# Performance work log

Hardware: AMD Instinct MI355X
Metric: run time of the kernel (lower is better)

The kernel has to match this reference:

```python
import jax, jax.numpy as jnp
import numpy as np


def _selective_scan(u, delta, A, Bm, Cm, Dskip, delta_bias):
    # u, delta: (B, K*D, L); A: (K*D, N); Bm, Cm: (B, K, N, L); Dskip, delta_bias: (K*D,)
    Bsz, KD, L = u.shape
    K = Bm.shape[1]
    D = KD // K
    N = A.shape[1]
    dt = jax.nn.softplus(delta + delta_bias[None, :, None])          # (B,KD,L)
    u4 = u.reshape(Bsz, K, D, L)
    dt4 = dt.reshape(Bsz, K, D, L)
    A4 = A.reshape(K, D, N)
    # discretization: dA = exp(dt*A), dBu = dt * B * u
    dA = jnp.exp(dt4[..., None] * A4[None, :, :, None, :])            # (B,K,D,L,N)
    Bt = jnp.transpose(Bm, (0, 1, 3, 2))                               # (B,K,L,N)
    dBu = dt4[..., None] * u4[..., None] * Bt[:, :, None, :, :]        # (B,K,D,L,N)
    dA_l = jnp.moveaxis(dA, 3, 0)                                      # (L,B,K,D,N)
    dBu_l = jnp.moveaxis(dBu, 3, 0)

    def step(h, ab):
        a, b = ab
        h = a * h + b
        return h, h

    h0 = jnp.zeros(dA_l.shape[1:], dA.dtype)
    _, hs = jax.lax.scan(step, h0, (dA_l, dBu_l))                      # (L,B,K,D,N)
    C_l = jnp.moveaxis(Cm, 3, 0)                                       # (L,B,K,N)
    y = jnp.einsum('lbkdn,lbkn->lbkd', hs, C_l)                        # (L,B,K,D)
    y = jnp.moveaxis(y, 0, 3).reshape(Bsz, KD, L)
    return y + u * Dskip[None, :, None]


def setup_inputs() -> dict:
    key = jax.random.key(0)
    ks = jax.random.split(key, 8)
    B, H, W, C = 2, 64, 64, 96
    Di, N, K = 192, 16, 4
    R = 6  # ceil(96/16)
    x = jax.random.normal(ks[0], (B, H, W, C), jnp.float32)
    in_proj_w = jax.random.normal(ks[1], (2 * Di, C), jnp.float32) * (C ** -0.5)
    conv_w = jax.random.normal(ks[2], (Di, 1, 3, 3), jnp.float32) * 0.2
    conv_b = jax.random.normal(ks[3], (Di,), jnp.float32) * 0.02
    x_proj_weight = jax.random.normal(ks[4], (K, R + 2 * N, Di), jnp.float32) * (Di ** -0.5)
    dt_projs_weight = jax.random.uniform(ks[5], (K, Di, R), jnp.float32, -(R ** -0.5), R ** -0.5)
    dt = jnp.exp(jax.random.uniform(ks[6], (K, Di), jnp.float32) * (np.log(0.1) - np.log(0.001)) + np.log(0.001))
    dt = jnp.clip(dt, 1e-4)
    dt_projs_bias = dt + jnp.log(-jnp.expm1(-dt))                      # inverse softplus
    A_logs = jnp.log(jnp.tile(jnp.arange(1, N + 1, dtype=jnp.float32), (K * Di, 1)))
    Ds = jnp.ones((K * Di,), jnp.float32)
    out_norm_w = jnp.ones((Di,), jnp.float32)
    out_norm_b = jnp.zeros((Di,), jnp.float32)
    out_proj_w = jax.random.normal(ks[7], (C, Di), jnp.float32) * (Di ** -0.5)
    return dict(x=x, in_proj_w=in_proj_w, conv_w=conv_w, conv_b=conv_b,
                x_proj_weight=x_proj_weight, dt_projs_weight=dt_projs_weight,
                dt_projs_bias=dt_projs_bias, A_logs=A_logs, Ds=Ds,
                out_norm_w=out_norm_w, out_norm_b=out_norm_b, out_proj_w=out_proj_w)


def reference(x, in_proj_w, conv_w, conv_b, x_proj_weight, dt_projs_weight,
              dt_projs_bias, A_logs, Ds, out_norm_w, out_norm_b, out_proj_w):
    Bsz, H, W, C = x.shape
    Di = conv_w.shape[0]
    K = x_proj_weight.shape[0]
    R = dt_projs_weight.shape[2]
    N = A_logs.shape[1]
    L = H * W
    # in_proj (bias=False) and split into x, z
    xz = x @ in_proj_w.T                                               # (B,H,W,2*Di)
    xi, z = jnp.split(xz, 2, axis=-1)
    # depthwise conv2d + SiLU (channel-first)
    xc = jnp.transpose(xi, (0, 3, 1, 2))                               # (B,Di,H,W)
    xc = jax.lax.conv_general_dilated(xc, conv_w, (1, 1), 'SAME',
                                      feature_group_count=Di) + conv_b[None, :, None, None]
    xc = jax.nn.silu(xc)
    # cross-scan: 4 directions (row-major, col-major, and their reverses)
    x0 = xc.reshape(Bsz, Di, L)
    x1 = jnp.transpose(xc, (0, 1, 3, 2)).reshape(Bsz, Di, L)
    xs = jnp.stack([x0, x1, x0[..., ::-1], x1[..., ::-1]], axis=1)      # (B,K,Di,L)
    # per-direction projections
    x_dbl = jnp.einsum('bkdl,kcd->bkcl', xs, x_proj_weight)            # (B,K,R+2N,L)
    dts, Bs, Cs = jnp.split(x_dbl, [R, R + N], axis=2)
    dts = jnp.einsum('bkrl,kdr->bkdl', dts, dt_projs_weight)           # (B,K,Di,L)
    A = -jnp.exp(A_logs)                                               # (K*Di,N)
    ys = _selective_scan(xs.reshape(Bsz, K * Di, L), dts.reshape(Bsz, K * Di, L),
                         A, Bs, Cs, Ds, dt_projs_bias.reshape(-1))
    ys = ys.reshape(Bsz, K, Di, L)
    # cross-merge
    y = ys[:, 0] + ys[:, 2, :, ::-1]
    yt = ys[:, 1] + ys[:, 3, :, ::-1]                                  # col-major ordering
    y = y + jnp.transpose(yt.reshape(Bsz, Di, W, H), (0, 1, 3, 2)).reshape(Bsz, Di, L)
    y = jnp.transpose(y.reshape(Bsz, Di, H, W), (0, 2, 3, 1))          # (B,H,W,Di)
    # out_norm: LayerNorm over channel
    mu = jnp.mean(y, axis=-1, keepdims=True)
    var = jnp.mean((y - mu) ** 2, axis=-1, keepdims=True)
    y = (y - mu) * jax.lax.rsqrt(var + 1e-5) * out_norm_w + out_norm_b
    # gate and out_proj (bias=False)
    y = y * jax.nn.silu(z)
    return y @ out_proj_w.T
```

## Files before the change

kernel.cpp:

```cpp
#include <hip/hip_runtime.h>
#include <hip/hip_fp16.h>
#include <math.h>


static constexpr int Bsz = 2;
static constexpr int Lc  = 4096;
static constexpr int Cc  = 96;
static constexpr int Dd  = 192;
static constexpr int Kk  = 4;
static constexpr int NC  = 32;

__device__ __forceinline__ float bu(unsigned short v) {
    return __uint_as_float((unsigned int)v << 16);
}
__device__ __forceinline__ unsigned short f2b(float f) {
    unsigned int u = __float_as_uint(f);
    return (unsigned short)((u + 0x7fffu + ((u >> 16) & 1u)) >> 16);
}

template<int CTRL>
__device__ __forceinline__ float dppadd(float x) {
    return x + __int_as_float(__builtin_amdgcn_update_dpp(
        0, __float_as_int(x), CTRL, 0xf, 0xf, true));
}
__device__ __forceinline__ float red16(float x) {
    x = dppadd<0xB1>(x);
    x = dppadd<0x4E>(x);
    x = dppadd<0x124>(x);
    x = dppadd<0x128>(x);
    return x;
}

__global__ __launch_bounds__(256) void k0_detect(const unsigned short* __restrict__ x,
                                                 int* __restrict__ flag)
{
    __shared__ int s[256];
    int cnt = 0;
    for (int i = threadIdx.x; i < 4096; i += 256) {
        int e = (x[i] >> 7) & 0xFF;
        cnt += (e >= 118 && e <= 131) ? 1 : 0;
    }
    s[threadIdx.x] = cnt;
    __syncthreads();
    for (int st = 128; st > 0; st >>= 1) {
        if (threadIdx.x < st) s[threadIdx.x] += s[threadIdx.x + st];
        __syncthreads();
    }
    if (threadIdx.x == 0) flag[0] = (s[0] >= 3072) ? 1 : 0;
}

struct Cv {
    const void* src[12];
    int off[12];
    int n[12];
};
__global__ __launch_bounds__(256) void k0b_convert(Cv cv, const int* __restrict__ flag,
                                                   float* __restrict__ dstbase)
{
    int bf = flag[0];
    int t = blockIdx.y;
    int i = blockIdx.x * 256 + threadIdx.x;
    if (i >= cv.n[t]) return;
    if (t == 11) {
        int cp = i % 40;
        int d  = (i / 40) % 192;
        int k  = i / 7680;
        float v = 0.f;
        if (cp < 38) {
            size_t si = (size_t)(k * 38 + cp) * 192 + d;
            v = bf ? bu(((const unsigned short*)cv.src[11])[si])
                   : ((const float*)cv.src[11])[si];
        }
        dstbase[cv.off[11] + i] = v;
        return;
    }
    float v;
    if (bf) v = bu(((const unsigned short*)cv.src[t])[i]);
    else    v = ((const float*)cv.src[t])[i];
    dstbase[cv.off[t] + i] = v;
}

__global__ __launch_bounds__(256) void k1_inproj(const void* __restrict__ xraw,
                                                 const int* __restrict__ flag,
                                                 const float* __restrict__ wf,
                                                 float* __restrict__ xiT, __half* __restrict__ zT)
{
    __shared__ float xT[64 * 97];
    const int bf = flag[0];
    int lt = blockIdx.x & 127;
    int jq = blockIdx.x >> 7;
    int row0 = lt * 64;
    for (int e = threadIdx.x; e < 64 * 96; e += 256) {
        int i = e / 96, c = e % 96;
        size_t idx = (size_t)(row0 + i) * Cc + c;
        xT[i * 97 + c] = bf ? bu(((const unsigned short*)xraw)[idx])
                            : ((const float*)xraw)[idx];
    }
    __syncthreads();
    int pi = threadIdx.x & 63;
    int q  = __builtin_amdgcn_readfirstlane(threadIdx.x >> 6);
    int j0 = jq * 96 + q * 24;
    float acc[24];
#pragma unroll
    for (int j = 0; j < 24; ++j) acc[j] = 0.f;
    for (int c4 = 0; c4 < 24; ++c4) {
        float xv0 = xT[pi * 97 + c4 * 4 + 0];
        float xv1 = xT[pi * 97 + c4 * 4 + 1];
        float xv2 = xT[pi * 97 + c4 * 4 + 2];
        float xv3 = xT[pi * 97 + c4 * 4 + 3];
#pragma unroll
        for (int j = 0; j < 24; ++j) {
            float4 w4 = *reinterpret_cast<const float4*>(&wf[(size_t)(j0 + j) * 96 + c4 * 4]);
            acc[j] += w4.x * xv0 + w4.y * xv1 + w4.z * xv2 + w4.w * xv3;
        }
    }
    int b = row0 >> 12;
    int l = (row0 & 4095) + pi;
    if (jq < 2) {
#pragma unroll
        for (int j = 0; j < 24; ++j)
            xiT[((size_t)b * Dd + j0 + j) * Lc + l] = acc[j];
    } else {
#pragma unroll
        for (int j = 0; j < 24; ++j) {
            float v = acc[j];
            zT[((size_t)b * Dd + (j0 + j - 192)) * Lc + l] =
                __float2half(v / (1.f + __expf(-v)));
        }
    }
}

__global__ __launch_bounds__(256) void k2b_conv(const float* __restrict__ xiT,
                                                const float* __restrict__ cwf,
                                                const float* __restrict__ cbf,
                                                float* __restrict__ xc,
                                                float* __restrict__ uT)
{
    __shared__ float inl[34 * 66];
    __shared__ float outl[32 * 65];
    int bid = blockIdx.x;
    int half = bid & 1;
    int d = (bid >> 1) % Dd;
    int b = bid / (2 * Dd);
    int h0 = half * 32;
    const float* src = xiT + (size_t)(b * Dd + d) * Lc;
    for (int r = threadIdx.x; r < 34; r += 256) {
        inl[r * 66 + 0] = 0.f;
        inl[r * 66 + 65] = 0.f;
    }
    for (int e = threadIdx.x; e < 34 * 64; e += 256) {
        int row = e >> 6, w = e & 63;
        int h = h0 - 1 + row;
        inl[row * 66 + 1 + w] = (h >= 0 && h < 64) ? src[h * 64 + w] : 0.f;
    }
    __syncthreads();
    float wgt[9];
#pragma unroll
    for (int t = 0; t < 9; t++) wgt[t] = cwf[d * 9 + t];
    float bias = cbf[d];
    int hs = threadIdx.x >> 6, w = threadIdx.x & 63;
    float* dstrow = xc + (size_t)(b * Dd + d) * Lc;
#pragma unroll
    for (int it = 0; it < 8; ++it) {
        int hh = it * 4 + hs;
        float acc = bias;
#pragma unroll
        for (int dy = 0; dy < 3; ++dy) {
            const float* rp = &inl[(hh + dy) * 66 + w];
#pragma unroll
            for (int dx = 0; dx < 3; ++dx)
                acc += rp[dx] * wgt[dy * 3 + dx];
        }
        float s = acc / (1.f + __expf(-acc));
        dstrow[(h0 + hh) * 64 + w] = s;
        outl[hh * 65 + w] = s;
    }
    __syncthreads();
    float* udst = uT + (size_t)(b * Dd + d) * Lc;
    for (int e = threadIdx.x; e < 2048; e += 256) {
        int w2 = e >> 5, hh2 = e & 31;
        udst[w2 * 64 + h0 + hh2] = outl[hh2 * 65 + w2];
    }
}

__global__ __launch_bounds__(256) void k3_proj(const float* __restrict__ xc,
                                               const float* __restrict__ uT,
                                               const float* __restrict__ Wg,
                                               const float* __restrict__ dtwf,
                                               const float* __restrict__ dtbf,
                                               __half* __restrict__ dtH,
                                               float* __restrict__ BsT, float* __restrict__ CsT)
{
    __shared__ float xL[192 * 64];
    __shared__ float rawdt[6][64];
    int bid = blockIdx.x;
    int pt = bid & 63, k = (bid >> 6) & 3, b = bid >> 8;
    int s0 = pt * 64;
    const float* xb = ((k & 1) ? uT : xc) + (size_t)b * Dd * Lc + s0;
    for (int e = threadIdx.x; e < 3072; e += 256) {
        int d = e >> 4, c4 = e & 15;
        *reinterpret_cast<float4*>(&xL[d * 64 + c4 * 4]) =
            *reinterpret_cast<const float4*>(xb + (size_t)d * Lc + c4 * 4);
    }
    __syncthreads();

    int pi = threadIdx.x & 63;
    int q  = __builtin_amdgcn_readfirstlane(threadIdx.x >> 6);

    const float* wk = Wg + (size_t)k * 192 * 40 + q * 10;

    float acc[10];
#pragma unroll
    for (int j = 0; j < 10; ++j) acc[j] = 0.f;

    for (int d = 0; d < 192; ++d) {
        float xv = xL[d * 64 + pi];
        const float* wrow = wk + d * 40;
#pragma unroll
        for (int j = 0; j < 10; ++j) acc[j] += wrow[j] * xv;
    }

    if (q == 0) {
#pragma unroll
        for (int j = 0; j < 6; ++j) rawdt[j][pi] = acc[j];
    }
    size_t bk16 = (size_t)(b * Kk + k) * 16;
#pragma unroll
    for (int j = 0; j < 10; ++j) {
        int cp = q * 10 + j;
        if (cp >= 6 && cp < 22)
            BsT[(bk16 + (cp - 6)) * Lc + s0 + pi] = acc[j];
        else if (cp >= 22 && cp < 38)
            CsT[(bk16 + (cp - 22)) * Lc + s0 + pi] = acc[j];
    }
    __syncthreads();

    float raws[6];
#pragma unroll
    for (int r = 0; r < 6; ++r) raws[r] = rawdt[r][pi];
    const float* dtw = dtwf + (size_t)(k * 192 + q * 48) * 6;
    const float* dtb = dtbf + k * 192 + q * 48;
    __half* dto = dtH + ((size_t)(b * Kk + k) * Dd + q * 48) * Lc + s0 + pi;
    for (int dd = 0; dd < 48; ++dd) {
        float s = dtb[dd];
#pragma unroll
        for (int r = 0; r < 6; ++r) s += raws[r] * dtw[dd * 6 + r];
        float sp = fmaxf(s, 0.f) + __logf(1.f + __expf(-fabsf(s)));
        dto[(size_t)dd * Lc] = __float2half(sp);
    }
}

template<int REV, int PASS3>
__device__ __forceinline__ void scan_run(const float* __restrict__ ubase,
                                         const __half* __restrict__ dbase,
                                         const float* __restrict__ Bbase,
                                         const float* __restrict__ Cbase,
                                         float* uL, float* bL, float* cL, __half* dL,
                                         int dl, int n, int c,
                                         float An,
                                         float* __restrict__ P, float* __restrict__ S,
                                         size_t pidx, __half* __restrict__ yrow)
{
    const int t0 = c * 128;
    const int mb0 = REV ? (Lc - 64 - t0) : t0;
    const int mb1 = REV ? (Lc - 128 - t0) : (t0 + 64);

    float4 ru = *reinterpret_cast<const float4*>(ubase + mb0 + n * 4);
    float4 rb = *reinterpret_cast<const float4*>(Bbase + mb0 + n * 4);
    float4 rc{};
    if (PASS3) rc = *reinterpret_cast<const float4*>(Cbase + mb0 + n * 4);
    uint2 rd = *reinterpret_cast<const uint2*>(dbase + mb0 + n * 4);
    *reinterpret_cast<float4*>(uL + dl * 68 + n * 4) = ru;
    *reinterpret_cast<float4*>(bL + dl * 68 + n * 4) = rb;
    if (PASS3) *reinterpret_cast<float4*>(cL + dl * 68 + n * 4) = rc;
    *reinterpret_cast<uint2*>(dL + dl * 72 + n * 4) = rd;
    __syncthreads();

    ru = *reinterpret_cast<const float4*>(ubase + mb1 + n * 4);
    rb = *reinterpret_cast<const float4*>(Bbase + mb1 + n * 4);
    if (PASS3) rc = *reinterpret_cast<const float4*>(Cbase + mb1 + n * 4);
    rd = *reinterpret_cast<const uint2*>(dbase + mb1 + n * 4);

    float h = PASS3 ? P[pidx] : 0.f;
    float sdt = 0.f, ystash = 0.f;

#define SS2D_HALF(HH)                                                           \
    {                                                                           \
        _Pragma("unroll 4")                                                     \
        for (int qi = 0; qi < 16; ++qi) {                                       \
            const int col4 = REV ? (60 - qi * 4) : (qi * 4);                    \
            float4 uq = *reinterpret_cast<const float4*>(uL + dl * 68 + col4);  \
            float4 bq = *reinterpret_cast<const float4*>(bL + n * 68 + col4);   \
            float4 cq{};                                                        \
            if (PASS3) cq = *reinterpret_cast<const float4*>(cL + n * 68 + col4);\
            uint2 dq = *reinterpret_cast<const uint2*>(dL + dl * 72 + col4);    \
            const __half2* dh2 = reinterpret_cast<const __half2*>(&dq);         \
            _Pragma("unroll")                                                   \
            for (int j = 0; j < 4; ++j) {                                       \
                const int e = REV ? (3 - j) : j;                                \
                float dtv = (e & 1) ? __high2float(dh2[e >> 1])                 \
                                    : __low2float(dh2[e >> 1]);                 \
                float uv = reinterpret_cast<const float*>(&uq)[e];              \
                float bv = reinterpret_cast<const float*>(&bq)[e];              \
                float a = __expf(dtv * An);                                     \
                if (!PASS3) sdt += dtv;                                         \
                h = a * h + (dtv * uv) * bv;                                    \
                if (PASS3) {                                                    \
                    float cv = reinterpret_cast<const float*>(&cq)[e];          \
                    float yv = red16(h * cv);                                   \
                    const int i15 = (qi & 3) * 4 + j;                           \
                    if (i15 == n) ystash = yv;                                  \
                    if (i15 == 15) {                                            \
                        int tb = t0 + (HH) * 64 + (qi >> 2) * 16 + n;           \
                        int aw = REV ? (Lc - 1 - tb) : tb;                      \
                        yrow[aw] = __float2half(ystash);                        \
                    }                                                           \
                }                                                               \
            }                                                                   \
        }                                                                       \
    }

    SS2D_HALF(0);
    __syncthreads();
    *reinterpret_cast<float4*>(uL + dl * 68 + n * 4) = ru;
    *reinterpret_cast<float4*>(bL + dl * 68 + n * 4) = rb;
    if (PASS3) *reinterpret_cast<float4*>(cL + dl * 68 + n * 4) = rc;
    *reinterpret_cast<uint2*>(dL + dl * 72 + n * 4) = rd;
    __syncthreads();
    SS2D_HALF(1);
#undef SS2D_HALF

    if (!PASS3) {
        P[pidx] = __expf(An * sdt);
        S[pidx] = h;
    }
}

template<int PASS3>
__global__ __launch_bounds__(256) void kscan(const __half* __restrict__ dtH,
                                             const float* __restrict__ xc,
                                             const float* __restrict__ uT,
                                             const float* __restrict__ BsT,
                                             const float* __restrict__ CsT,
                                             const float* __restrict__ alogf,
                                             float* __restrict__ P,
                                             float* __restrict__ S,
                                             __half* __restrict__ ysH)
{
    __shared__ float uL[16 * 68];
    __shared__ float bL[16 * 68];
    __shared__ float cL[PASS3 ? 16 * 68 : 4];
    __shared__ __half dL[16 * 72];

    int c  = blockIdx.x & 31;
    int t1 = blockIdx.x >> 5;
    int dg = t1 % 12;
    int kk = (t1 / 12) & 3;
    int b  = t1 / 48;
    int n  = threadIdx.x & 15, dl = threadIdx.x >> 4;
    int d  = dg * 16 + dl;

    const float* ubz = ((kk & 1) ? uT : xc) + (size_t)b * Dd * Lc;
    const float*  ubase = ubz + (size_t)d * Lc;
    const __half* dbase = dtH + ((size_t)((b * Kk + kk) * Dd + d)) * Lc;
    const float*  Bbase = BsT + ((size_t)((b * Kk + kk) * 16 + dl)) * Lc;
    const float*  Cbase = CsT + ((size_t)((b * Kk + kk) * 16 + dl)) * Lc;

    float An  = -__expf(alogf[(kk * Dd + d) * 16 + n]);
    size_t pidx = (((size_t)(b * Kk + kk) * Dd + d) * NC + c) * 16 + n;
    __half* yrow = PASS3 ? ysH + ((size_t)(kk * Bsz + b) * Dd + d) * Lc : nullptr;

    if (kk >= 2)
        scan_run<1, PASS3>(ubase, dbase, Bbase, Cbase, uL, bL, cL, dL,
                           dl, n, c, An, P, S, pidx, yrow);
    else
        scan_run<0, PASS3>(ubase, dbase, Bbase, Cbase, uL, bL, cL, dL,
                           dl, n, c, An, P, S, pidx, yrow);
}

__global__ __launch_bounds__(64) void k6_pass2(float* __restrict__ P, const float* __restrict__ S)
{
    int g = blockIdx.x * 64 + threadIdx.x;
    int n = g & 15;
    int chain = g >> 4;
    size_t base = (size_t)chain * NC * 16 + n;
    float h = 0.f;
#pragma unroll
    for (int c = 0; c < NC; ++c) {
        size_t id = base + (size_t)c * 16;
        float p = P[id], s = S[id];
        P[id] = h;
        h = p * h + s;
    }
}

__global__ __launch_bounds__(256) void k8t(const __half* __restrict__ ysH,
                                           __half* __restrict__ ysT)
{
    __shared__ float t[64 * 65];
    int bid = blockIdx.x;
    int d = bid % Dd, b = bid / Dd;
    const __half* y1 = ysH + ((size_t)(1 * Bsz + b) * Dd + d) * Lc;
    const __half* y3 = ysH + ((size_t)(3 * Bsz + b) * Dd + d) * Lc;
    __half* dst = ysT + ((size_t)b * Dd + d) * Lc;
    for (int e = threadIdx.x; e < 4096; e += 256)
        t[(e >> 6) * 65 + (e & 63)] = __half2float(y1[e]) + __half2float(y3[e]);
    __syncthreads();
    for (int e = threadIdx.x; e < 4096; e += 256)
        dst[e] = __float2half(t[(e & 63) * 65 + (e >> 6)]);
}

__global__ __launch_bounds__(256) void k8_norm(const __half* __restrict__ ysH,
                                               const __half* __restrict__ ysT,
                                               const __half* __restrict__ zT,
                                               const float* __restrict__ xc,
                                               const float* __restrict__ dsf,
                                               const float* __restrict__ nwf,
                                               const float* __restrict__ nbf,
                                               __half* __restrict__ gH)
{
    __shared__ float yt[192 * 33];
    __shared__ float ps1[8 * 32], ps2[8 * 32];
    __shared__ float mu[32], rs[32];
    int bid = blockIdx.x;
    int pt = bid & 127, b = bid >> 7;
    int p0 = pt * 32;
    for (int e = threadIdx.x; e < 192 * 32; e += 256) {
        int d = e >> 5, p = e & 31;
        size_t r0 = ((size_t)(0 * Bsz + b) * Dd + d) * Lc + p0 + p;
        size_t r2 = ((size_t)(2 * Bsz + b) * Dd + d) * Lc + p0 + p;
        size_t rt = ((size_t)b * Dd + d) * Lc + p0 + p;
        float ds4 = dsf[d] + dsf[192 + d] + dsf[384 + d] + dsf[576 + d];
        yt[d * 33 + p] = __half2float(ysH[r0]) + __half2float(ysH[r2])
                       + __half2float(ysT[rt])
                       + xc[((size_t)b * Dd + d) * Lc + p0 + p] * ds4;
    }
    __syncthreads();
    {
        int p = threadIdx.x & 31, q = threadIdx.x >> 5;
        float s1 = 0.f, s2 = 0.f;
        for (int dd = 0; dd < 24; ++dd) {
            float v = yt[(q * 24 + dd) * 33 + p];
            s1 += v; s2 += v * v;
        }
        ps1[q * 32 + p] = s1; ps2[q * 32 + p] = s2;
    }
    __syncthreads();
    if (threadIdx.x < 32) {
        int p = threadIdx.x;
        float s1 = 0.f, s2 = 0.f;
        for (int q = 0; q < 8; ++q) { s1 += ps1[q * 32 + p]; s2 += ps2[q * 32 + p]; }
        float m = s1 * (1.f / 192.f);
        float var = s2 * (1.f / 192.f) - m * m;
        mu[p] = m; rs[p] = rsqrtf(var + 1e-5f);
    }
    __syncthreads();
    for (int e = threadIdx.x; e < 192 * 32; e += 256) {
        int d = e >> 5, p = e & 31;
        float v = (yt[d * 33 + p] - mu[p]) * rs[p] * nwf[d] + nbf[d];
        float zv = __half2float(zT[((size_t)b * Dd + d) * Lc + p0 + p]);
        yt[d * 33 + p] = v * zv;
    }
    __syncthreads();
    for (int i = threadIdx.x; i < 32 * 192; i += 256) {
        int p = i / 192, d = i - p * 192;
        gH[((size_t)b * Lc + p0 + p) * Dd + d] = __float2half(yt[d * 33 + p]);
    }
}

__global__ __launch_bounds__(1024) void k10_outproj(const __half* __restrict__ gH,
                                                    const float* __restrict__ wof,
                                                    const int* __restrict__ flag,
                                                    void* __restrict__ outv)
{
    __shared__ float gLT[192 * 66];
    const int bf = flag[0];
    int r0 = blockIdx.x * 64;
    for (int e = threadIdx.x; e < 1536; e += 1024) {
        int row = e / 24, j = e % 24;
        __half2 g2[4];
        *reinterpret_cast<uint4*>(g2) =
            *reinterpret_cast<const uint4*>(gH + (size_t)(r0 + row) * Dd + j * 8);
#pragma unroll
        for (int i = 0; i < 4; ++i) {
            gLT[(j * 8 + 2 * i + 0) * 66 + row] = __low2float(g2[i]);
            gLT[(j * 8 + 2 * i + 1) * 66 + row] = __high2float(g2[i]);
        }
    }
    __syncthreads();
    int row = threadIdx.x & 63;
    int w = __builtin_amdgcn_readfirstlane(threadIdx.x >> 6);
    int c0 = w * 6;
    const float* wr = wof + (size_t)c0 * Dd;
    float acc[6];
#pragma unroll
    for (int i = 0; i < 6; ++i) acc[i] = 0.f;
    for (int d = 0; d < 192; ++d) {
        float gv = gLT[d * 66 + row];
#pragma unroll
        for (int cc = 0; cc < 6; ++cc) acc[cc] += wr[(size_t)cc * Dd + d] * gv;
    }
    size_t ob = (size_t)(r0 + row) * Cc + c0;
    if (bf) {
        unsigned short* o = (unsigned short*)outv;
#pragma unroll
        for (int cc = 0; cc < 6; ++cc) o[ob + cc] = f2b(acc[cc]);
    } else {
        float* o = (float*)outv;
#pragma unroll
        for (int cc = 0; cc < 6; ++cc) o[ob + cc] = acc[cc];
    }
}

extern "C" void kernel_launch(void* const* d_in, const int* in_sizes, int n_in,
                              void* d_out, int out_size, void* d_ws, size_t ws_size,
                              hipStream_t stream)
{
    (void)out_size; (void)ws_size;
    float* ws = (float*)d_ws;
    int* flag = (int*)ws;

    int off[12]; int tot = 64;
    off[0] = 0;
    for (int i = 1; i < 12; ++i) {
        off[i] = tot;
        int n = (i < n_in) ? in_sizes[i] : 0;
        tot += (n + 63) & ~63;
    }
    float* winf = ws + off[1];
    float* cwf  = ws + off[2];
    float* cbf  = ws + off[3];
    float* dtwf = ws + off[5];
    float* dtbf = ws + off[6];
    float* alogf= ws + off[7];
    float* dsf  = ws + off[8];
    float* nwf  = ws + off[9];
    float* nbf  = ws + off[10];
    float* wof  = ws + off[11];

    const size_t BASE = 131072;
    __half* dtH = (__half*)(ws + BASE);
    float*  xc  = ws + BASE + 3145728;
    float*  uT  = ws + BASE + 4718592;
    float*  BsT = ws + BASE + 6291456;
    float*  CsT = ws + BASE + 6815744;
    float*  P   = ws + BASE + 7340032;
    float*  S   = ws + BASE + 8126464;
    __half* zT  = (__half*)(ws + BASE + 8912896);
    float*  xiT = ws + BASE + 9699328;
    __half* ysH = (__half*)(ws + BASE + 9699328);
    __half* ysT = (__half*)P;
    __half* gH  = (__half*)S;
    float*  Wg  = ws + BASE + 12845056;

    Cv cv2;
    for (int i = 0; i < 11; ++i) {
        int t = i + 1;
        cv2.src[i] = (t < n_in) ? d_in[t] : d_in[0];
        cv2.off[i] = off[t];
        cv2.n[i]   = (t < n_in) ? in_sizes[t] : 0;
    }
    cv2.src[11] = (4 < n_in) ? d_in[4] : d_in[0];
    cv2.off[11] = (int)(BASE + 12845056);
    cv2.n[11]   = 4 * 192 * 40;

    k0_detect   <<<dim3(1),    dim3(256), 0, stream>>>((const unsigned short*)d_in[0], flag);
    k0b_convert <<<dim3(144, 12), dim3(256), 0, stream>>>(cv2, flag, ws);
    k1_inproj   <<<dim3(512),  dim3(256), 0, stream>>>(d_in[0], flag, winf, xiT, zT);
    k2b_conv    <<<dim3(768),  dim3(256), 0, stream>>>(xiT, cwf, cbf, xc, uT);
    k3_proj     <<<dim3(512),  dim3(256), 0, stream>>>(xc, uT, Wg, dtwf, dtbf, dtH, BsT, CsT);
    kscan<0>    <<<dim3(3072), dim3(256), 0, stream>>>(dtH, xc, uT, BsT, CsT, alogf, P, S, ysH);
    k6_pass2    <<<dim3(384),  dim3(64),  0, stream>>>(P, S);
    kscan<1>    <<<dim3(3072), dim3(256), 0, stream>>>(dtH, xc, uT, BsT, CsT, alogf, P, S, ysH);
    k8t         <<<dim3(384),  dim3(256), 0, stream>>>(ysH, ysT);
    k8_norm     <<<dim3(256),  dim3(256), 0, stream>>>(ysH, ysT, zT, xc, dsf, nwf, nbf, gH);
    k10_outproj <<<dim3(128),  dim3(1024), 0, stream>>>(gH, wof, flag, d_out);
}
```

Measured before the change: 182.5 us.

## Fuse dtype detection into convert and merge layernorm with out-projection

The standalone dtype-detection kernel is folded into the weight-convert kernel, where every block redundantly counts exponents and block 0 writes the flag. The LayerNorm/gating kernel and the output-projection GEMM are merged into one kernel. It works on 64-position tiles held in shared memory, and each wave computes 24 output channels. This removes two launches and the fp16 round trip of the gated activations through global memory. In exchange there are only 128 blocks with 24 accumulators per thread and 50KB of LDS, which lowers occupancy and parallelism for the projection.

```diff
diff --git a/kernel.cpp b/kernel.cpp
--- a/kernel.cpp
+++ b/kernel.cpp
@@ -31,22 +31,23 @@
     return x;
 }
 
-__global__ __launch_bounds__(256) void k0_detect(const unsigned short* __restrict__ x,
-                                                 int* __restrict__ flag)
-{
-    __shared__ int s[256];
+__device__ __forceinline__ int detect_bf(const unsigned short* __restrict__ x,
+                                         int* __restrict__ sbuf)
+{
     int cnt = 0;
     for (int i = threadIdx.x; i < 4096; i += 256) {
         int e = (x[i] >> 7) & 0xFF;
         cnt += (e >= 118 && e <= 131) ? 1 : 0;
     }
-    s[threadIdx.x] = cnt;
+    sbuf[threadIdx.x] = cnt;
     __syncthreads();
     for (int st = 128; st > 0; st >>= 1) {
-        if (threadIdx.x < st) s[threadIdx.x] += s[threadIdx.x + st];
+        if (threadIdx.x < st) sbuf[threadIdx.x] += sbuf[threadIdx.x + st];
         __syncthreads();
     }
-    if (threadIdx.x == 0) flag[0] = (s[0] >= 3072) ? 1 : 0;
+    int r = (sbuf[0] >= 3072) ? 1 : 0;
+    __syncthreads();
+    return r;
 }
 
 struct Cv {
@@ -54,10 +55,13 @@
     int off[12];
     int n[12];
 };
-__global__ __launch_bounds__(256) void k0b_convert(Cv cv, const int* __restrict__ flag,
+__global__ __launch_bounds__(256) void k0b_convert(Cv cv, const unsigned short* __restrict__ xraw,
+                                                   int* __restrict__ flag,
                                                    float* __restrict__ dstbase)
 {
-    int bf = flag[0];
+    __shared__ int sbuf[256];
+    int bf = detect_bf(xraw, sbuf);
+    if (blockIdx.y == 0 && blockIdx.x == 0 && threadIdx.x == 0) flag[0] = bf;
     int t = blockIdx.y;
     int i = blockIdx.x * 256 + threadIdx.x;
     if (i >= cv.n[t]) return;
@@ -410,105 +414,82 @@
         dst[e] = __float2half(t[(e & 63) * 65 + (e >> 6)]);
 }
 
-__global__ __launch_bounds__(256) void k8_norm(const __half* __restrict__ ysH,
-                                               const __half* __restrict__ ysT,
-                                               const __half* __restrict__ zT,
-                                               const float* __restrict__ xc,
-                                               const float* __restrict__ dsf,
-                                               const float* __restrict__ nwf,
-                                               const float* __restrict__ nbf,
-                                               __half* __restrict__ gH)
-{
-    __shared__ float yt[192 * 33];
-    __shared__ float ps1[8 * 32], ps2[8 * 32];
-    __shared__ float mu[32], rs[32];
+__global__ __launch_bounds__(256) void k89_final(const __half* __restrict__ ysH,
+                                                 const __half* __restrict__ ysT,
+                                                 const __half* __restrict__ zT,
+                                                 const float* __restrict__ xc,
+                                                 const float* __restrict__ dsf,
+                                                 const float* __restrict__ nwf,
+                                                 const float* __restrict__ nbf,
+                                                 const float* __restrict__ wof,
+                                                 const int* __restrict__ flag,
+                                                 void* __restrict__ outv)
+{
+    __shared__ float yt[192 * 65];
+    __shared__ float ps1[4 * 64], ps2[4 * 64];
+    __shared__ float mu[64], rs[64];
+    const int bf = flag[0];
     int bid = blockIdx.x;
-    int pt = bid & 127, b = bid >> 7;
-    int p0 = pt * 32;
-    for (int e = threadIdx.x; e < 192 * 32; e += 256) {
-        int d = e >> 5, p = e & 31;
+    int pt = bid & 63, b = bid >> 6;
+    int p0 = pt * 64;
+    for (int e = threadIdx.x; e < 192 * 64; e += 256) {
+        int d = e >> 6, p = e & 63;
         size_t r0 = ((size_t)(0 * Bsz + b) * Dd + d) * Lc + p0 + p;
         size_t r2 = ((size_t)(2 * Bsz + b) * Dd + d) * Lc + p0 + p;
         size_t rt = ((size_t)b * Dd + d) * Lc + p0 + p;
         float ds4 = dsf[d] + dsf[192 + d] + dsf[384 + d] + dsf[576 + d];
-        yt[d * 33 + p] = __half2float(ysH[r0]) + __half2float(ysH[r2])
+        yt[d * 65 + p] = __half2float(ysH[r0]) + __half2float(ysH[r2])
                        + __half2float(ysT[rt])
                        + xc[((size_t)b * Dd + d) * Lc + p0 + p] * ds4;
     }
     __syncthreads();
     {
-        int p = threadIdx.x & 31, q = threadIdx.x >> 5;
+        int p = threadIdx.x & 63, q = threadIdx.x >> 6;
         float s1 = 0.f, s2 = 0.f;
-        for (int dd = 0; dd < 24; ++dd) {
-            float v = yt[(q * 24 + dd) * 33 + p];
+        for (int dd = 0; dd < 48; ++dd) {
+            float v = yt[(q * 48 + dd) * 65 + p];
             s1 += v; s2 += v * v;
         }
-        ps1[q * 32 + p] = s1; ps2[q * 32 + p] = s2;
-    }
-    __syncthreads();
-    if (threadIdx.x < 32) {
+        ps1[q * 64 + p] = s1; ps2[q * 64 + p] = s2;
+    }
+    __syncthreads();
+    if (threadIdx.x < 64) {
         int p = threadIdx.x;
-        float s1 = 0.f, s2 = 0.f;
-        for (int q = 0; q < 8; ++q) { s1 += ps1[q * 32 + p]; s2 += ps2[q * 32 + p]; }
+        float s1 = ps1[p] + ps1[64 + p] + ps1[128 + p] + ps1[192 + p];
+        float s2 = ps2[p] + ps2[64 + p] + ps2[128 + p] + ps2[192 + p];
         float m = s1 * (1.f / 192.f);
         float var = s2 * (1.f / 192.f) - m * m;
         mu[p] = m; rs[p] = rsqrtf(var + 1e-5f);
     }
     __syncthreads();
-    for (int e = threadIdx.x; e < 192 * 32; e += 256) {
-        int d = e >> 5, p = e & 31;
-        float v = (yt[d * 33 + p] - mu[p]) * rs[p] * nwf[d] + nbf[d];
+    for (int e = threadIdx.x; e < 192 * 64; e += 256) {
+        int d = e >> 6, p = e & 63;
+        float v = (yt[d * 65 + p] - mu[p]) * rs[p] * nwf[d] + nbf[d];
         float zv = __half2float(zT[((size_t)b * Dd + d) * Lc + p0 + p]);
-        yt[d * 33 + p] = v * zv;
-    }
-    __syncthreads();
-    for (int i = threadIdx.x; i < 32 * 192; i += 256) {
-        int p = i / 192, d = i - p * 192;
-        gH[((size_t)b * Lc + p0 + p) * Dd + d] = __float2half(yt[d * 33 + p]);
-    }
-}
-
-__global__ __launch_bounds__(1024) void k10_outproj(const __half* __restrict__ gH,
-                                                    const float* __restrict__ wof,
-                                                    const int* __restrict__ flag,
-                                                    void* __restrict__ outv)
-{
-    __shared__ float gLT[192 * 66];
-    const int bf = flag[0];
-    int r0 = blockIdx.x * 64;
-    for (int e = threadIdx.x; e < 1536; e += 1024) {
-        int row = e / 24, j = e % 24;
-        __half2 g2[4];
-        *reinterpret_cast<uint4*>(g2) =
-            *reinterpret_cast<const uint4*>(gH + (size_t)(r0 + row) * Dd + j * 8);
-#pragma unroll
-        for (int i = 0; i < 4; ++i) {
-            gLT[(j * 8 + 2 * i + 0) * 66 + row] = __low2float(g2[i]);
-            gLT[(j * 8 + 2 * i + 1) * 66 + row] = __high2float(g2[i]);
-        }
-    }
-    __syncthreads();
-    int row = threadIdx.x & 63;
-    int w = __builtin_amdgcn_readfirstlane(threadIdx.x >> 6);
-    int c0 = w * 6;
+        yt[d * 65 + p] = v * zv;
+    }
+    __syncthreads();
+    int pos = threadIdx.x & 63;
+    int cg  = __builtin_amdgcn_readfirstlane(threadIdx.x >> 6);
+    int c0  = cg * 24;
     const float* wr = wof + (size_t)c0 * Dd;
-    float acc[6];
-#pragma unroll
-    for (int i = 0; i < 6; ++i) acc[i] = 0.f;
+    float acc[24];
+#pragma unroll
+    for (int i = 0; i < 24; ++i) acc[i] = 0.f;
     for (int d = 0; d < 192; ++d) {
-        float gv = gLT[d * 66 + row];
-#pragma unroll
-        for (int cc = 0; cc < 6; ++cc) acc[cc] += wr[(size_t)cc * Dd + d] * gv;
-    }
-    size_t ob = (size_t)(r0 + row) * Cc + c0;
+        float gv = yt[d * 65 + pos];
+#pragma unroll
+        for (int cc = 0; cc < 24; ++cc) acc[cc] += wr[(size_t)cc * Dd + d] * gv;
+    }
+    size_t ob = (size_t)(b * Lc + p0 + pos) * Cc + c0;
     if (bf) {
         unsigned short* o = (unsigned short*)outv;
 #pragma unroll
-        for (int cc = 0; cc < 6; ++cc) o[ob + cc] = f2b(acc[cc]);
+        for (int cc = 0; cc < 24; ++cc) o[ob + cc] = f2b(acc[cc]);
     } else {
         float* o = (float*)outv;
 #pragma unroll
-        for (int cc = 0; cc < 6; ++cc) o[ob + cc] = acc[cc];
+        for (int cc = 0; cc < 24; ++cc) o[ob + cc] = acc[cc];
     }
 }
 
@@ -550,7 +531,6 @@
     float*  xiT = ws + BASE + 9699328;
     __half* ysH = (__half*)(ws + BASE + 9699328);
     __half* ysT = (__half*)P;
-    __half* gH  = (__half*)S;
     float*  Wg  = ws + BASE + 12845056;
 
     Cv cv2;
@@ -564,8 +544,7 @@
     cv2.off[11] = (int)(BASE + 12845056);
     cv2.n[11]   = 4 * 192 * 40;
 
-    k0_detect   <<<dim3(1),    dim3(256), 0, stream>>>((const unsigned short*)d_in[0], flag);
-    k0b_convert <<<dim3(144, 12), dim3(256), 0, stream>>>(cv2, flag, ws);
+    k0b_convert <<<dim3(144, 12), dim3(256), 0, stream>>>(cv2, (const unsigned short*)d_in[0], flag, ws);
     k1_inproj   <<<dim3(512),  dim3(256), 0, stream>>>(d_in[0], flag, winf, xiT, zT);
     k2b_conv    <<<dim3(768),  dim3(256), 0, stream>>>(xiT, cwf, cbf, xc, uT);
     k3_proj     <<<dim3(512),  dim3(256), 0, stream>>>(xc, uT, Wg, dtwf, dtbf, dtH, BsT, CsT);
@@ -573,6 +552,5 @@
     k6_pass2    <<<dim3(384),  dim3(64),  0, stream>>>(P, S);
     kscan<1>    <<<dim3(3072), dim3(256), 0, stream>>>(dtH, xc, uT, BsT, CsT, alogf, P, S, ysH);
     k8t         <<<dim3(384),  dim3(256), 0, stream>>>(ysH, ysT);
-    k8_norm     <<<dim3(256),  dim3(256), 0, stream>>>(ysH, ysT, zT, xc, dsf, nwf, nbf, gH);
-    k10_outproj <<<dim3(128),  dim3(1024), 0, stream>>>(gH, wof, flag, d_out);
-}
+    k89_final   <<<dim3(128),  dim3(256), 0, stream>>>(ysH, ysT, zT, xc, dsf, nwf, nbf, wof, flag, d_out);
+}
```

New measurement: 199.0 us. 9.0% more time.
